# Kernel tuning notes

Hardware: AMD Instinct MI355X
Metric: run time of the kernel (lower is better)

## Reference

```python
import jax, jax.numpy as jnp
import numpy as np

V, E, H, ENC, ATT = 10000, 256, 512, 512, 512
B, S, NF, MAXLEN = 128, 25, 196, 64


def setup_inputs() -> dict:
    key = jax.random.key(0)
    ks = jax.random.split(key, 24)
    g = lambda k, shp: (jax.random.normal(k, shp, dtype=jnp.float32) * 0.05)
    emb = g(ks[0], (V, E)).at[0].set(0.0)  # padding_idx=0 row zeroed
    return {
        'decoder_input': jax.random.randint(ks[1], (B, S), 0, V, dtype=jnp.int32),
        'encoder_outputs': jax.random.normal(ks[2], (B, NF, ENC), dtype=jnp.float32),
        'emb': emb,
        'pos_emb': g(ks[3], (MAXLEN, E)),
        'Uw': g(ks[4], (ATT, ENC)), 'Ub': g(ks[5], (ATT,)),
        'Ww': g(ks[6], (ATT, H)), 'Wb': g(ks[7], (ATT,)),
        'Aw': g(ks[8], (1, ATT)), 'Ab': g(ks[9], (1,)),
        'init_h_w': g(ks[10], (H, ENC)), 'init_h_b': g(ks[11], (H,)),
        'init_c_w': g(ks[12], (H, ENC)), 'init_c_b': g(ks[13], (H,)),
        'W_ih': g(ks[14], (4 * H, E + ENC)), 'W_hh': g(ks[15], (4 * H, H)),
        'b_ih': g(ks[16], (4 * H,)), 'b_hh': g(ks[17], (4 * H,)),
        'fcn_w': g(ks[18], (V, H)), 'fcn_b': g(ks[19], (V,)),
    }


def reference(decoder_input, encoder_outputs, emb, pos_emb, Uw, Ub, Ww, Wb, Aw, Ab,
              init_h_w, init_h_b, init_c_w, init_c_b, W_ih, W_hh, b_ih, b_hh,
              fcn_w, fcn_b):
    # Loop-invariant attention key projection: U(features) -> [B, NF, ATT]
    u_hs = jnp.einsum('bne,ae->bna', encoder_outputs, Uw) + Ub
    mean_enc = encoder_outputs.mean(axis=1)                  # [B, ENC]
    h0 = mean_enc @ init_h_w.T + init_h_b                    # [B, H]
    c0 = mean_enc @ init_c_w.T + init_c_b
    tokens = decoder_input.T                                 # [S, B]
    positions = jnp.arange(tokens.shape[0])

    def step(carry, inp):
        h, c = carry
        tok, pos = inp
        embeds = emb[tok] + pos_emb[pos]                     # [B, E]
        w_ah = h @ Ww.T + Wb                                 # [B, ATT]
        scores = jnp.tanh(u_hs + w_ah[:, None, :]) @ Aw[0] + Ab[0]  # [B, NF]
        alpha = jax.nn.softmax(scores, axis=1)
        context = jnp.einsum('bnd,bn->bd', encoder_outputs, alpha)  # [B, ENC]
        x = jnp.concatenate([embeds, context], axis=1)       # [B, E+ENC]
        gates = x @ W_ih.T + b_ih + h @ W_hh.T + b_hh        # [B, 4H]
        i, f, g_, o = jnp.split(gates, 4, axis=1)
        c_new = jax.nn.sigmoid(f) * c + jax.nn.sigmoid(i) * jnp.tanh(g_)
        h_new = jax.nn.sigmoid(o) * jnp.tanh(c_new)
        out = h_new @ fcn_w.T + fcn_b                        # [B, V] (dropout=eval identity)
        return (h_new, c_new), (out, alpha)

    _, (outs, alphas) = jax.lax.scan(step, (h0, c0), (tokens, positions))
    return outs.transpose(1, 0, 2), alphas.transpose(1, 0, 2)
```

## Files before the change

### kernel.cpp

```cpp
#include <hip/hip_runtime.h>

constexpr int B_ = 128, S_ = 25, NF_ = 196, ENC_ = 512, ATT_ = 512;
constexpr int H_ = 512, E_ = 256, V_ = 10000, G4_ = 2048;
constexpr int VPAD_ = 10112;

typedef __attribute__((ext_vector_type(8))) __bf16 bf16x8;
typedef __attribute__((ext_vector_type(4))) __bf16 bf16x4;
typedef __attribute__((ext_vector_type(4))) float f32x4;

__device__ __forceinline__ float bflo(unsigned u) {
    return __builtin_bit_cast(float, u << 16);
}
__device__ __forceinline__ float bfhi(unsigned u) {
    return __builtin_bit_cast(float, u & 0xffff0000u);
}
__device__ __forceinline__ float fast_tanhf(float x) {
    x = fminf(fmaxf(x, -15.f), 15.f);
    return 1.f - 2.f * __fdividef(1.f, __expf(2.f * x) + 1.f);
}
__device__ __forceinline__ float fast_sigf(float x) {
    x = fminf(fmaxf(x, -30.f), 30.f);
    return __fdividef(1.f, 1.f + __expf(-x));
}

__device__ __forceinline__ int gperm(int n) {
    int j = (n & 15) + ((n >> 6) << 4);
    int g = (n >> 4) & 3;
    return g * 512 + j;
}

__global__ __launch_bounds__(256) void k_cvt(const float* __restrict__ s,
                                             __bf16* __restrict__ d, int n4) {
    int i = blockIdx.x * 256 + threadIdx.x;
    if (i >= n4) return;
    float4 v = *(const float4*)&s[(size_t)i * 4];
    bf16x4 o;
    o[0] = (__bf16)v.x; o[1] = (__bf16)v.y; o[2] = (__bf16)v.z; o[3] = (__bf16)v.w;
    *(bf16x4*)&d[(size_t)i * 4] = o;
}

__global__ __launch_bounds__(256) void k_cvt_fcw(const float* __restrict__ s,
                                                 __bf16* __restrict__ d) {
    int i = blockIdx.x * 256 + threadIdx.x;
    if (i >= VPAD_ * 512 / 4) return;
    int e = i * 4;
    int row = e >> 9;
    bf16x4 o;
    if (row < V_) {
        float4 v = *(const float4*)&s[(size_t)row * 512 + (e & 511)];
        o[0] = (__bf16)v.x; o[1] = (__bf16)v.y; o[2] = (__bf16)v.z; o[3] = (__bf16)v.w;
    } else {
        o[0] = o[1] = o[2] = o[3] = (__bf16)0.f;
    }
    *(bf16x4*)&d[(size_t)e] = o;
}

__global__ __launch_bounds__(256) void k_pack_ww(const float* __restrict__ Ww,
                                                 unsigned* __restrict__ W2) {
    __shared__ float Ts[32][65];
    int t = threadIdx.x;
    int k0 = blockIdx.x * 32, j0 = blockIdx.y * 64;
    int c = t & 31, rr = t >> 5;
#pragma unroll
    for (int i = 0; i < 8; ++i) {
        int j = j0 + rr + i * 8;
        Ts[c][rr + i * 8] = Ww[(size_t)j * 512 + k0 + c];
    }
    __syncthreads();
#pragma unroll
    for (int i = 0; i < 4; ++i) {
        int kr = (t >> 5) + i * 8;
        int jc = t & 31;
        __bf16 b0 = (__bf16)Ts[kr][2 * jc], b1 = (__bf16)Ts[kr][2 * jc + 1];
        unsigned u = (unsigned)__builtin_bit_cast(unsigned short, b0)
                   | ((unsigned)__builtin_bit_cast(unsigned short, b1) << 16);
        W2[(size_t)(k0 + kr) * 256 + (j0 >> 1) + jc] = u;
    }
}

__global__ __launch_bounds__(256) void k_cvt_wih_r(const float* __restrict__ W_ih,
                                                   __bf16* __restrict__ o) {
    int n = blockIdx.x, k = threadIdx.x;
    int row = gperm(n);
    o[(size_t)n * 256 + k] = (__bf16)W_ih[(size_t)row * 768 + k];
}

__global__ __launch_bounds__(256) void k_pack_wcat(const float* __restrict__ W_ih,
                                                   const float* __restrict__ W_hh,
                                                   __bf16* __restrict__ Wcat) {
    int n = blockIdx.x, t = threadIdx.x;
    int row = gperm(n);
#pragma unroll
    for (int i = 0; i < 4; ++i) {
        int k = t + i * 256;
        float v = (k < 512) ? W_ih[(size_t)row * 768 + 256 + k]
                            : W_hh[(size_t)row * 512 + (k - 512)];
        Wcat[(size_t)n * 1024 + k] = (__bf16)v;
    }
}

__global__ __launch_bounds__(256) void k_pack_biasr(const float* __restrict__ b_ih,
                                                    const float* __restrict__ b_hh,
                                                    float* __restrict__ bsum_r) {
    int n = blockIdx.x * 256 + threadIdx.x;
    int row = gperm(n);
    bsum_r[n] = b_ih[row] + b_hh[row];
}

__global__ __launch_bounds__(256) void k_embed(const int* __restrict__ dec,
                                               const float* __restrict__ emb,
                                               const float* __restrict__ pose,
                                               __bf16* __restrict__ out) {
    int bx = blockIdx.x;
    int s = bx >> 7, b = bx & 127;
    int e = threadIdx.x;
    int tok = dec[b * S_ + s];
    out[(size_t)bx * E_ + e] = (__bf16)(emb[tok * E_ + e] + pose[s * E_ + e]);
}

__global__ __launch_bounds__(1024) void k_init2(const float* __restrict__ enc,
                                                const float* __restrict__ ihw, const float* __restrict__ ihb,
                                                const float* __restrict__ icw, const float* __restrict__ icb,
                                                __bf16* __restrict__ Abuf0, float* __restrict__ cbuf) {
    __shared__ float pm[1024];
    __shared__ __align__(16) float mean[512];
    int b = blockIdx.x, t = threadIdx.x;
    int d = t & 511, q = t >> 9;
    const float* ep = enc + ((size_t)b * 196 + q * 98) * 512 + d;
    float sum = 0.f;
#pragma unroll 7
    for (int n = 0; n < 98; ++n) sum += ep[(size_t)n * 512];
    pm[t] = sum;
    __syncthreads();
    if (t < 512) mean[t] = (pm[t] + pm[t + 512]) * (1.f / 196.f);
    __syncthreads();
    int w = t >> 6, ln = t & 63;
    float4 m4a = *(const float4*)&mean[ln * 8];
    float4 m4b = *(const float4*)&mean[ln * 8 + 4];
#pragma unroll 4
    for (int i = 0; i < 32; ++i) {
        int j = i * 16 + w;
        const float4* wh = (const float4*)&ihw[(size_t)j * 512 + ln * 8];
        const float4* wc = (const float4*)&icw[(size_t)j * 512 + ln * 8];
        float4 ha = wh[0], hb = wh[1], ca = wc[0], cb = wc[1];
        float ah = m4a.x * ha.x + m4a.y * ha.y + m4a.z * ha.z + m4a.w * ha.w
                 + m4b.x * hb.x + m4b.y * hb.y + m4b.z * hb.z + m4b.w * hb.w;
        float ac = m4a.x * ca.x + m4a.y * ca.y + m4a.z * ca.z + m4a.w * ca.w
                 + m4b.x * cb.x + m4b.y * cb.y + m4b.z * cb.z + m4b.w * cb.w;
#pragma unroll
        for (int off = 32; off; off >>= 1) {
            ah += __shfl_xor(ah, off);
            ac += __shfl_xor(ac, off);
        }
        if (ln == 0) {
            Abuf0[(size_t)b * 1024 + 512 + j] = (__bf16)(ah + ihb[j]);
            cbuf[b * 512 + j] = ac + icb[j];
        }
    }
}

template<int MODE>
__global__ __launch_bounds__(256) void k_mfma_gemm(
    const __bf16* __restrict__ A, int lda, const __bf16* __restrict__ Bm,
    const float* __restrict__ bias1, void* __restrict__ Cout,
    int K, int Nreal, int ldc) {
    __shared__ __align__(16) __bf16 As[128 * 64];
    __shared__ __align__(16) __bf16 Bs[128 * 64];
    int tid = threadIdx.x;
    int lane = tid & 63, w = tid >> 6;
    int m0 = blockIdx.x * 128, n0 = blockIdx.y * 128;
    int wm = (w & 1) * 64, wn = (w >> 1) * 64;
    f32x4 acc[4][4] = {};
    int srow = tid >> 3;
    int ke = (tid & 7) * 8;
    int kgw = tid & 7;

    for (int k0 = 0; k0 < K; k0 += 64) {
#pragma unroll
        for (int it = 0; it < 4; ++it) {
            int row = it * 32 + srow;
            bf16x8 av = *(const bf16x8*)(A + (size_t)(m0 + row) * lda + k0 + ke);
            bf16x8 bv = *(const bf16x8*)(Bm + (size_t)(n0 + row) * K + k0 + ke);
            int kg = kgw ^ (row & 7);
            *(bf16x8*)&As[row * 64 + kg * 8] = av;
            *(bf16x8*)&Bs[row * 64 + kg * 8] = bv;
        }
        __syncthreads();
        bf16x8 af[4][2], bfr[4][2];
#pragma unroll
        for (int f = 0; f < 4; ++f) {
#pragma unroll
            for (int ks = 0; ks < 2; ++ks) {
                int ra = wm + f * 16 + (lane & 15);
                int rb = wn + f * 16 + (lane & 15);
                int kgl = ks * 4 + (lane >> 4);
                af[f][ks]  = *(const bf16x8*)&As[ra * 64 + (kgl ^ (ra & 7)) * 8];
                bfr[f][ks] = *(const bf16x8*)&Bs[rb * 64 + (kgl ^ (rb & 7)) * 8];
            }
        }
#pragma unroll
        for (int fm = 0; fm < 4; ++fm)
#pragma unroll
            for (int fn = 0; fn < 4; ++fn)
#pragma unroll
                for (int ks = 0; ks < 2; ++ks)
                    acc[fm][fn] = __builtin_amdgcn_mfma_f32_16x16x32_bf16(
                        af[fm][ks], bfr[fn][ks], acc[fm][fn], 0, 0, 0);
        __syncthreads();
    }
    int cm = (lane >> 4) * 4, cn = lane & 15;
#pragma unroll
    for (int fm = 0; fm < 4; ++fm) {
#pragma unroll
        for (int fn = 0; fn < 4; ++fn) {
#pragma unroll
            for (int r = 0; r < 4; ++r) {
                int gm = m0 + wm + fm * 16 + cm + r;
                int gn = n0 + wn + fn * 16 + cn;
                float v = acc[fm][fn][r];
                if (MODE == 0) {
                    if (gn < Nreal) {
                        int orow = (gm & 127) * S_ + (gm >> 7);
                        ((float*)Cout)[(size_t)orow * ldc + gn] = v + bias1[gn];
                    }
                } else {
                    ((__bf16*)Cout)[(size_t)gm * ldc + gn] = (__bf16)(v + bias1[gn]);
                }
            }
        }
    }
}

__global__ __launch_bounds__(1024) void k_attn2(
    const __bf16* __restrict__ u_hs,
    const unsigned* __restrict__ enc2,
    const unsigned* __restrict__ W2,
    const float* __restrict__ Wb, const float* __restrict__ Aw,
    __bf16* __restrict__ Abuf,
    float* __restrict__ alphas, int s) {
    __shared__ __align__(16) float hs[512];
    __shared__ float wah[512];
    __shared__ float pc[2048];
    __shared__ float sc[200];
    __shared__ float red[256];
    __shared__ float al[200];
    int b = blockIdx.x, t = threadIdx.x;
    int ln = t & 63, w = t >> 6;

    if (t < 256) {
        unsigned u = ((const unsigned*)Abuf)[b * 512 + 256 + t];
        hs[2 * t] = bflo(u); hs[2 * t + 1] = bfhi(u);
    }
    __syncthreads();
    {
        int jp = t & 255, kq = t >> 8;
        float a0 = 0.f, a1 = 0.f;
        const unsigned* wp = W2 + (size_t)(kq * 128) * 256 + jp;
        const float4* h4 = (const float4*)(hs + kq * 128);
#pragma unroll 4
        for (int k4 = 0; k4 < 32; ++k4) {
            float4 hk = h4[k4];
            unsigned w0 = wp[(k4 * 4 + 0) * 256];
            unsigned w1 = wp[(k4 * 4 + 1) * 256];
            unsigned w2 = wp[(k4 * 4 + 2) * 256];
            unsigned w3 = wp[(k4 * 4 + 3) * 256];
            a0 += hk.x * bflo(w0); a1 += hk.x * bfhi(w0);
            a0 += hk.y * bflo(w1); a1 += hk.y * bfhi(w1);
            a0 += hk.z * bflo(w2); a1 += hk.z * bfhi(w2);
            a0 += hk.w * bflo(w3); a1 += hk.w * bfhi(w3);
        }
        pc[kq * 512 + 2 * jp] = a0;
        pc[kq * 512 + 2 * jp + 1] = a1;
    }
    __syncthreads();
    if (t < 512)
        wah[t] = pc[t] + pc[512 + t] + pc[1024 + t] + pc[1536 + t] + Wb[t];
    __syncthreads();
    {
        float av[8], wv[8];
#pragma unroll
        for (int i = 0; i < 8; ++i) { av[i] = Aw[ln * 8 + i]; wv[i] = wah[ln * 8 + i]; }
        for (int n = w; n < NF_; n += 16) {
            bf16x8 u8 = *(const bf16x8*)(u_hs + ((size_t)(b * NF_ + n)) * 512 + ln * 8);
            float acc = 0.f;
#pragma unroll
            for (int i = 0; i < 8; ++i)
                acc += fast_tanhf((float)u8[i] + wv[i]) * av[i];
#pragma unroll
            for (int off = 32; off; off >>= 1) acc += __shfl_xor(acc, off);
            if (ln == 0) sc[n] = acc;
        }
    }
    __syncthreads();
    if (t < 256) red[t] = (t < NF_) ? sc[t] : -1e30f;
    __syncthreads();
#pragma unroll
    for (int off = 128; off; off >>= 1) {
        if (t < off) red[t] = fmaxf(red[t], red[t + off]);
        __syncthreads();
    }
    float mx = red[0];
    __syncthreads();
    float e = (t < NF_) ? __expf(sc[t] - mx) : 0.f;
    if (t < 256) red[t] = e;
    __syncthreads();
#pragma unroll
    for (int off = 128; off; off >>= 1) {
        if (t < off) red[t] += red[t + off];
        __syncthreads();
    }
    float inv = __fdividef(1.f, red[0]);
    __syncthreads();
    if (t < NF_) {
        float a = e * inv;
        al[t] = a;
        alphas[((size_t)b * S_ + s) * NF_ + t] = a;
    }
    __syncthreads();
    {
        int p2 = t & 255, q2 = t >> 8;
        float c0 = 0.f, c1 = 0.f;
        for (int i = q2; i < NF_; i += 4) {
            unsigned u = enc2[((size_t)(b * NF_ + i)) * 256 + p2];
            float a = al[i];
            c0 += a * bflo(u); c1 += a * bfhi(u);
        }
        pc[q2 * 512 + 2 * p2] = c0;
        pc[q2 * 512 + 2 * p2 + 1] = c1;
    }
    __syncthreads();
    if (t < 512)
        Abuf[(size_t)b * 1024 + t] =
            (__bf16)(pc[t] + pc[512 + t] + pc[1024 + t] + pc[1536 + t]);
}

__global__ __launch_bounds__(256) void k_gates(
    const __bf16* __restrict__ Abuf,
    const __bf16* __restrict__ Wcat,
    const __bf16* __restrict__ gatespre,
    float* __restrict__ cbuf,
    __bf16* __restrict__ AbufN,
    __bf16* __restrict__ Hall_bf,
    int s) {
    __shared__ __align__(16) __bf16 As[2][32 * 64];
    __shared__ __align__(16) __bf16 Bs[2][64 * 64];
    __shared__ float Red[2048];
    int tid = threadIdx.x;
    int lane = tid & 63, w = tid >> 6;
    int m0 = blockIdx.x * 32, n0 = blockIdx.y * 64;
    int kh = w >> 1, wm = (w & 1) * 16;
    f32x4 acc[4] = {};
    int srow = tid >> 3;
    int ke = (tid & 7) * 8;
    int kgw = tid & 7;

    for (int k0 = 0; k0 < 512; k0 += 64) {
#pragma unroll
        for (int h = 0; h < 2; ++h) {
            int kb = h * 512 + k0;
            bf16x8 av = *(const bf16x8*)(Abuf + (size_t)(m0 + srow) * 1024 + kb + ke);
            int kg = kgw ^ (srow & 7);
            *(bf16x8*)&As[h][srow * 64 + kg * 8] = av;
#pragma unroll
            for (int it = 0; it < 2; ++it) {
                int row = it * 32 + srow;
                bf16x8 bv = *(const bf16x8*)(Wcat + (size_t)(n0 + row) * 1024 + kb + ke);
                int kg2 = kgw ^ (row & 7);
                *(bf16x8*)&Bs[h][row * 64 + kg2 * 8] = bv;
            }
        }
        __syncthreads();
        bf16x8 af[2], bfr[4][2];
#pragma unroll
        for (int ks = 0; ks < 2; ++ks) {
            int ra = wm + (lane & 15);
            int kgl = ks * 4 + (lane >> 4);
            af[ks] = *(const bf16x8*)&As[kh][ra * 64 + ((kgl ^ (ra & 7))) * 8];
#pragma unroll
            for (int fn = 0; fn < 4; ++fn) {
                int rb = fn * 16 + (lane & 15);
                bfr[fn][ks] = *(const bf16x8*)&Bs[kh][rb * 64 + ((kgl ^ (rb & 7))) * 8];
            }
        }
#pragma unroll
        for (int fn = 0; fn < 4; ++fn)
#pragma unroll
            for (int ks = 0; ks < 2; ++ks)
                acc[fn] = __builtin_amdgcn_mfma_f32_16x16x32_bf16(
                    af[ks], bfr[fn][ks], acc[fn], 0, 0, 0);
        __syncthreads();
    }
    int base = ((w & 1) * 64 + lane) * 16;
    if (kh == 1) {
#pragma unroll
        for (int fn = 0; fn < 4; ++fn)
#pragma unroll
            for (int r = 0; r < 4; ++r) Red[base + fn * 4 + r] = acc[fn][r];
    }
    __syncthreads();
    if (kh == 0) {
#pragma unroll
        for (int fn = 0; fn < 4; ++fn)
#pragma unroll
            for (int r = 0; r < 4; ++r) acc[fn][r] += Red[base + fn * 4 + r];
        int cm = (lane >> 4) * 4, cn = lane & 15;
        int j = (n0 >> 6) * 16 + cn;
#pragma unroll
        for (int r = 0; r < 4; ++r) {
            int b = m0 + wm + cm + r;
            const __bf16* gp = gatespre + ((size_t)(s * B_ + b)) * G4_ + n0 + cn;
            float qi = acc[0][r] + (float)gp[0];
            float qf = acc[1][r] + (float)gp[16];
            float qg = acc[2][r] + (float)gp[32];
            float qo = acc[3][r] + (float)gp[48];
            float ig = fast_sigf(qi), fg = fast_sigf(qf);
            float gg = fast_tanhf(qg), og = fast_sigf(qo);
            int ci = b * 512 + j;
            float cnew = fg * cbuf[ci] + ig * gg;
            float hn = og * fast_tanhf(cnew);
            cbuf[ci] = cnew;
            __bf16 hb = (__bf16)hn;
            AbufN[(size_t)b * 1024 + 512 + j] = hb;
            Hall_bf[(size_t)(s + 1) * 65536 + ci] = hb;
        }
    }
}

extern "C" void kernel_launch(void* const* d_in, const int* in_sizes, int n_in,
                              void* d_out, int out_size, void* d_ws, size_t ws_size,
                              hipStream_t stream) {
    const int*   dec  = (const int*)d_in[0];
    const float* enc  = (const float*)d_in[1];
    const float* emb  = (const float*)d_in[2];
    const float* pose = (const float*)d_in[3];
    const float* Uw   = (const float*)d_in[4];
    const float* Ub   = (const float*)d_in[5];
    const float* Ww   = (const float*)d_in[6];
    const float* Wb   = (const float*)d_in[7];
    const float* Aw   = (const float*)d_in[8];
    const float* ihw  = (const float*)d_in[10];
    const float* ihb  = (const float*)d_in[11];
    const float* icw  = (const float*)d_in[12];
    const float* icb  = (const float*)d_in[13];
    const float* W_ih = (const float*)d_in[14];
    const float* W_hh = (const float*)d_in[15];
    const float* b_ih = (const float*)d_in[16];
    const float* b_hh = (const float*)d_in[17];
    const float* fcw  = (const float*)d_in[18];
    const float* fcb  = (const float*)d_in[19];
    float* out = (float*)d_out;
    char*  wsb = (char*)d_ws;

    size_t o = 0;
    __bf16*   enc_bf   = (__bf16*)(wsb + o); o += (size_t)25088 * 512 * 2;
    __bf16*   u_hs_bf  = (__bf16*)(wsb + o); o += (size_t)25088 * 512 * 2;
    __bf16*   gpre_bf  = (__bf16*)(wsb + o); o += (size_t)3200 * 2048 * 2;
    __bf16*   Hall_bf  = (__bf16*)(wsb + o); o += (size_t)26 * 65536 * 2;
    float*    cbuf     = (float*)(wsb + o);  o += (size_t)65536 * 4;
    __bf16*   Abuf     = (__bf16*)(wsb + o); o += (size_t)2 * 128 * 1024 * 2;
    __bf16*   Uw_bf    = (__bf16*)(wsb + o); o += (size_t)262144 * 2;
    unsigned* W2       = (unsigned*)(wsb + o); o += (size_t)512 * 256 * 4;
    __bf16*   WihE_r   = (__bf16*)(wsb + o); o += (size_t)2048 * 256 * 2;
    __bf16*   embeds_bf= (__bf16*)(wsb + o); o += (size_t)3200 * 256 * 2;
    __bf16*   Wcat     = (__bf16*)(wsb + o); o += (size_t)2048 * 1024 * 2;
    float*    bsum_r   = (float*)(wsb + o);  o += (size_t)2048 * 4;
    __bf16*   fcw_bf   = (__bf16*)(wsb + o); o += (size_t)VPAD_ * 512 * 2;

    k_cvt<<<12544, 256, 0, stream>>>(enc, enc_bf, 3211264);
    k_cvt<<<256, 256, 0, stream>>>(Uw, Uw_bf, 65536);
    k_pack_ww<<<dim3(16, 8), 256, 0, stream>>>(Ww, W2);
    k_cvt_wih_r<<<2048, 256, 0, stream>>>(W_ih, WihE_r);
    k_pack_wcat<<<2048, 256, 0, stream>>>(W_ih, W_hh, Wcat);
    k_pack_biasr<<<8, 256, 0, stream>>>(b_ih, b_hh, bsum_r);
    k_embed<<<S_ * B_, 256, 0, stream>>>(dec, emb, pose, embeds_bf);
    k_init2<<<B_, 1024, 0, stream>>>(enc, ihw, ihb, icw, icb, Abuf, cbuf);
    k_cvt_fcw<<<5056, 256, 0, stream>>>(fcw, fcw_bf);

    k_mfma_gemm<1><<<dim3(196, 4), 256, 0, stream>>>(enc_bf, 512, Uw_bf, Ub,
                                                     u_hs_bf, 512, 512, 512);
    k_mfma_gemm<1><<<dim3(25, 16), 256, 0, stream>>>(embeds_bf, 256, WihE_r, bsum_r,
                                                     gpre_bf, 256, 2048, 2048);

    for (int s = 0; s < S_; ++s) {
        __bf16* Ap = Abuf + (size_t)(s & 1) * 131072;
        __bf16* An = Abuf + (size_t)((s + 1) & 1) * 131072;
        k_attn2<<<B_, 1024, 0, stream>>>(u_hs_bf, (const unsigned*)enc_bf, W2, Wb, Aw,
                                         Ap, out + 32000000, s);
        k_gates<<<dim3(4, 32), 256, 0, stream>>>(Ap, Wcat, gpre_bf, cbuf, An, Hall_bf, s);
    }

    k_mfma_gemm<0><<<dim3(25, 79), 256, 0, stream>>>(Hall_bf + 65536, 512, fcw_bf, fcb,
                                                     out, 512, V_, V_);
}
```

Measured before the change: 1.426 ms.

## Split attention over feature halves with deferred softmax normalization in gates kernel

The attention kernel is split across two blocks per batch row, each handling 98 features with 512 threads. The softmax max-reduction is dropped: each block writes unnormalized exp scores, partial sums and partial context vectors. The gates kernel then combines the two halves, normalizes the context and alphas, and loads the context directly into shared memory. This removes the serial max/sum reduction barriers and doubles the block count for the latency-bound attention step. The trade-offs are a redundant W·h projection in both blocks, extra global traffic for the partial results, and overflow risk from computing exp without subtracting the max.

```diff
diff --git a/kernel.cpp b/kernel.cpp
--- a/kernel.cpp
+++ b/kernel.cpp
@@ -231,20 +231,20 @@
     }
 }
 
-__global__ __launch_bounds__(1024) void k_attn2(
+__global__ __launch_bounds__(512) void k_attn3(
     const __bf16* __restrict__ u_hs,
     const unsigned* __restrict__ enc2,
     const unsigned* __restrict__ W2,
     const float* __restrict__ Wb, const float* __restrict__ Aw,
-    __bf16* __restrict__ Abuf,
-    float* __restrict__ alphas, int s) {
+    const __bf16* __restrict__ Abuf,
+    float* __restrict__ pctx,
+    float* __restrict__ lpart,
+    float* __restrict__ esg) {
     __shared__ __align__(16) float hs[512];
     __shared__ float wah[512];
-    __shared__ float pc[2048];
-    __shared__ float sc[200];
-    __shared__ float red[256];
-    __shared__ float al[200];
-    int b = blockIdx.x, t = threadIdx.x;
+    __shared__ float pc[1024];
+    __shared__ float es[100];
+    int b = blockIdx.x, hh = blockIdx.y, t = threadIdx.x;
     int ln = t & 63, w = t >> 6;
 
     if (t < 256) {
@@ -253,12 +253,12 @@
     }
     __syncthreads();
     {
-        int jp = t & 255, kq = t >> 8;
+        int jp = t & 255, q = t >> 8;
         float a0 = 0.f, a1 = 0.f;
-        const unsigned* wp = W2 + (size_t)(kq * 128) * 256 + jp;
-        const float4* h4 = (const float4*)(hs + kq * 128);
+        const unsigned* wp = W2 + (size_t)(q * 256) * 256 + jp;
+        const float4* h4 = (const float4*)(hs + q * 256);
 #pragma unroll 4
-        for (int k4 = 0; k4 < 32; ++k4) {
+        for (int k4 = 0; k4 < 64; ++k4) {
             float4 hk = h4[k4];
             unsigned w0 = wp[(k4 * 4 + 0) * 256];
             unsigned w1 = wp[(k4 * 4 + 1) * 256];
@@ -269,18 +269,18 @@
             a0 += hk.z * bflo(w2); a1 += hk.z * bfhi(w2);
             a0 += hk.w * bflo(w3); a1 += hk.w * bfhi(w3);
         }
-        pc[kq * 512 + 2 * jp] = a0;
-        pc[kq * 512 + 2 * jp + 1] = a1;
-    }
-    __syncthreads();
-    if (t < 512)
-        wah[t] = pc[t] + pc[512 + t] + pc[1024 + t] + pc[1536 + t] + Wb[t];
+        pc[q * 512 + 2 * jp] = a0;
+        pc[q * 512 + 2 * jp + 1] = a1;
+    }
+    __syncthreads();
+    wah[t] = pc[t] + pc[512 + t] + Wb[t];
     __syncthreads();
     {
         float av[8], wv[8];
 #pragma unroll
         for (int i = 0; i < 8; ++i) { av[i] = Aw[ln * 8 + i]; wv[i] = wah[ln * 8 + i]; }
-        for (int n = w; n < NF_; n += 16) {
+        for (int nl = w; nl < 98; nl += 8) {
+            int n = hh * 98 + nl;
             bf16x8 u8 = *(const bf16x8*)(u_hs + ((size_t)(b * NF_ + n)) * 512 + ln * 8);
             float acc = 0.f;
 #pragma unroll
@@ -288,85 +288,90 @@
                 acc += fast_tanhf((float)u8[i] + wv[i]) * av[i];
 #pragma unroll
             for (int off = 32; off; off >>= 1) acc += __shfl_xor(acc, off);
-            if (ln == 0) sc[n] = acc;
-        }
-    }
-    __syncthreads();
-    if (t < 256) red[t] = (t < NF_) ? sc[t] : -1e30f;
-    __syncthreads();
-#pragma unroll
-    for (int off = 128; off; off >>= 1) {
-        if (t < off) red[t] = fmaxf(red[t], red[t + off]);
-        __syncthreads();
-    }
-    float mx = red[0];
-    __syncthreads();
-    float e = (t < NF_) ? __expf(sc[t] - mx) : 0.f;
-    if (t < 256) red[t] = e;
-    __syncthreads();
-#pragma unroll
-    for (int off = 128; off; off >>= 1) {
-        if (t < off) red[t] += red[t + off];
-        __syncthreads();
-    }
-    float inv = __fdividef(1.f, red[0]);
-    __syncthreads();
-    if (t < NF_) {
-        float a = e * inv;
-        al[t] = a;
-        alphas[((size_t)b * S_ + s) * NF_ + t] = a;
+            if (ln == 0) es[nl] = __expf(acc);
+        }
     }
     __syncthreads();
     {
         int p2 = t & 255, q2 = t >> 8;
         float c0 = 0.f, c1 = 0.f;
-        for (int i = q2; i < NF_; i += 4) {
-            unsigned u = enc2[((size_t)(b * NF_ + i)) * 256 + p2];
-            float a = al[i];
+        for (int i = q2; i < 98; i += 2) {
+            unsigned u = enc2[((size_t)(b * NF_ + hh * 98 + i)) * 256 + p2];
+            float a = es[i];
             c0 += a * bflo(u); c1 += a * bfhi(u);
         }
         pc[q2 * 512 + 2 * p2] = c0;
         pc[q2 * 512 + 2 * p2 + 1] = c1;
     }
     __syncthreads();
-    if (t < 512)
-        Abuf[(size_t)b * 1024 + t] =
-            (__bf16)(pc[t] + pc[512 + t] + pc[1024 + t] + pc[1536 + t]);
-}
-
-__global__ __launch_bounds__(256) void k_gates(
+    pctx[((size_t)(hh * 128 + b)) * 512 + t] = pc[t] + pc[512 + t];
+    if (t < 98) esg[b * 256 + hh * 98 + t] = es[t];
+    if (t < 64) {
+        float v = es[t] + ((t + 64 < 98) ? es[t + 64] : 0.f);
+#pragma unroll
+        for (int off = 32; off; off >>= 1) v += __shfl_xor(v, off);
+        if (t == 0) lpart[hh * 128 + b] = v;
+    }
+}
+
+__global__ __launch_bounds__(256) void k_gates2(
     const __bf16* __restrict__ Abuf,
     const __bf16* __restrict__ Wcat,
     const __bf16* __restrict__ gatespre,
     float* __restrict__ cbuf,
     __bf16* __restrict__ AbufN,
     __bf16* __restrict__ Hall_bf,
-    int s) {
-    __shared__ __align__(16) __bf16 As[2][32 * 64];
+    const float* __restrict__ pctx, const float* __restrict__ lpart,
+    const float* __restrict__ esg, float* __restrict__ alphas, int s) {
+    __shared__ __align__(16) __bf16 ctxL[32 * 512];
+    __shared__ __align__(16) __bf16 As[32 * 64];
     __shared__ __align__(16) __bf16 Bs[2][64 * 64];
     __shared__ float Red[2048];
+    __shared__ float invs[32];
     int tid = threadIdx.x;
     int lane = tid & 63, w = tid >> 6;
     int m0 = blockIdx.x * 32, n0 = blockIdx.y * 64;
     int kh = w >> 1, wm = (w & 1) * 16;
-    f32x4 acc[4] = {};
     int srow = tid >> 3;
     int ke = (tid & 7) * 8;
     int kgw = tid & 7;
 
+    if (tid < 32) invs[tid] = __fdividef(1.f, lpart[m0 + tid] + lpart[128 + m0 + tid]);
+    __syncthreads();
+    for (int q = tid; q < 8192; q += 256) {
+        int row = q >> 8;
+        int kk = (q & 255) * 2;
+        float2 v0 = *(const float2*)&pctx[((size_t)(m0 + row)) * 512 + kk];
+        float2 v1 = *(const float2*)&pctx[((size_t)(128 + m0 + row)) * 512 + kk];
+        float iv = invs[row];
+        int base = row * 512 + (kk & ~63) + ((((kk >> 3) & 7) ^ (row & 7)) << 3) + (kk & 7);
+        ctxL[base] = (__bf16)((v0.x + v1.x) * iv);
+        ctxL[base + 1] = (__bf16)((v0.y + v1.y) * iv);
+    }
+    if (blockIdx.y == 0) {
+        for (int q = tid; q < 32 * 256; q += 256) {
+            int row = q >> 8, n = q & 255;
+            if (n < NF_)
+                alphas[((size_t)(m0 + row) * S_ + s) * NF_ + n] =
+                    esg[(m0 + row) * 256 + n] * invs[row];
+        }
+    }
+    __syncthreads();
+
+    f32x4 acc[4] = {};
     for (int k0 = 0; k0 < 512; k0 += 64) {
-#pragma unroll
-        for (int h = 0; h < 2; ++h) {
-            int kb = h * 512 + k0;
-            bf16x8 av = *(const bf16x8*)(Abuf + (size_t)(m0 + srow) * 1024 + kb + ke);
-            int kg = kgw ^ (srow & 7);
-            *(bf16x8*)&As[h][srow * 64 + kg * 8] = av;
-#pragma unroll
-            for (int it = 0; it < 2; ++it) {
-                int row = it * 32 + srow;
-                bf16x8 bv = *(const bf16x8*)(Wcat + (size_t)(n0 + row) * 1024 + kb + ke);
-                int kg2 = kgw ^ (row & 7);
-                *(bf16x8*)&Bs[h][row * 64 + kg2 * 8] = bv;
+        {
+            bf16x8 av = *(const bf16x8*)(Abuf + (size_t)(m0 + srow) * 1024 + 512 + k0 + ke);
+            *(bf16x8*)&As[srow * 64 + (kgw ^ (srow & 7)) * 8] = av;
+#pragma unroll
+            for (int h = 0; h < 2; ++h) {
+                int kb = h * 512 + k0;
+#pragma unroll
+                for (int it = 0; it < 2; ++it) {
+                    int row = it * 32 + srow;
+                    bf16x8 bv = *(const bf16x8*)(Wcat + (size_t)(n0 + row) * 1024 + kb + ke);
+                    *(bf16x8*)&Bs[h][row * 64 + (kgw ^ (row & 7)) * 8] = bv;
+                }
             }
         }
         __syncthreads();
@@ -375,7 +380,10 @@
         for (int ks = 0; ks < 2; ++ks) {
             int ra = wm + (lane & 15);
             int kgl = ks * 4 + (lane >> 4);
-            af[ks] = *(const bf16x8*)&As[kh][ra * 64 + ((kgl ^ (ra & 7))) * 8];
+            if (kh == 0)
+                af[ks] = *(const bf16x8*)&ctxL[ra * 512 + k0 + ((kgl ^ (ra & 7))) * 8];
+            else
+                af[ks] = *(const bf16x8*)&As[ra * 64 + ((kgl ^ (ra & 7))) * 8];
 #pragma unroll
             for (int fn = 0; fn < 4; ++fn) {
                 int rb = fn * 16 + (lane & 15);
@@ -465,6 +473,9 @@
     __bf16*   Wcat     = (__bf16*)(wsb + o); o += (size_t)2048 * 1024 * 2;
     float*    bsum_r   = (float*)(wsb + o);  o += (size_t)2048 * 4;
     __bf16*   fcw_bf   = (__bf16*)(wsb + o); o += (size_t)VPAD_ * 512 * 2;
+    float*    pctx     = (float*)(wsb + o);  o += (size_t)2 * 128 * 512 * 4;
+    float*    lpart    = (float*)(wsb + o);  o += (size_t)256 * 4;
+    float*    esg      = (float*)(wsb + o);  o += (size_t)128 * 256 * 4;
 
     k_cvt<<<12544, 256, 0, stream>>>(enc, enc_bf, 3211264);
     k_cvt<<<256, 256, 0, stream>>>(Uw, Uw_bf, 65536);
@@ -484,9 +495,10 @@
     for (int s = 0; s < S_; ++s) {
         __bf16* Ap = Abuf + (size_t)(s & 1) * 131072;
         __bf16* An = Abuf + (size_t)((s + 1) & 1) * 131072;
-        k_attn2<<<B_, 1024, 0, stream>>>(u_hs_bf, (const unsigned*)enc_bf, W2, Wb, Aw,
-                                         Ap, out + 32000000, s);
-        k_gates<<<dim3(4, 32), 256, 0, stream>>>(Ap, Wcat, gpre_bf, cbuf, An, Hall_bf, s);
+        k_attn3<<<dim3(B_, 2), 512, 0, stream>>>(u_hs_bf, (const unsigned*)enc_bf, W2,
+                                                 Wb, Aw, Ap, pctx, lpart, esg);
+        k_gates2<<<dim3(4, 32), 256, 0, stream>>>(Ap, Wcat, gpre_bf, cbuf, An, Hall_bf,
+                                                  pctx, lpart, esg, out + 32000000, s);
     }
 
     k_mfma_gemm<0><<<dim3(25, 79), 256, 0, stream>>>(Hall_bf + 65536, 512, fcw_bf, fcb,
```

After: 1.765 ms. 23.7% more time.

## Drop softmax max-subtraction and tree reductions; remap GEMM tiles across XCDs

Applied to the files above, without the earlier changes.

The attention kernel now exponentiates scores directly with no max subtraction. Each wavefront computes the softmax sum with shuffles, and the normalisation is deferred onto the context output. This removes two shared-memory tree reductions and many __syncthreads per step. Skipping the max is safe only while the scores stay small enough not to overflow, which holds for the bounded tanh·Aw sums here. Separately, MODE 0 GEMM blocks are remapped so that neighbouring tiles land on the same XCD, which is meant to improve L2 reuse.

```diff
diff --git a/kernel.cpp b/kernel.cpp
--- a/kernel.cpp
+++ b/kernel.cpp
@@ -168,7 +168,19 @@
     __shared__ __align__(16) __bf16 Bs[128 * 64];
     int tid = threadIdx.x;
     int lane = tid & 63, w = tid >> 6;
-    int m0 = blockIdx.x * 128, n0 = blockIdx.y * 128;
+    int m0, n0;
+    if (MODE == 0) {
+        int nwg = gridDim.x * gridDim.y;
+        int bid = blockIdx.y * gridDim.x + blockIdx.x;
+        int q = nwg >> 3, r = nwg & 7;
+        int xcd = bid & 7, lid = bid >> 3;
+        int wgid = (xcd < r) ? xcd * (q + 1) + lid : r * (q + 1) + (xcd - r) * q + lid;
+        m0 = (wgid % gridDim.x) * 128;
+        n0 = (wgid / gridDim.x) * 128;
+    } else {
+        m0 = blockIdx.x * 128;
+        n0 = blockIdx.y * 128;
+    }
     int wm = (w & 1) * 64, wn = (w >> 1) * 64;
     f32x4 acc[4][4] = {};
     int srow = tid >> 3;
@@ -242,8 +254,6 @@
     __shared__ float wah[512];
     __shared__ float pc[2048];
     __shared__ float sc[200];
-    __shared__ float red[256];
-    __shared__ float al[200];
     int b = blockIdx.x, t = threadIdx.x;
     int ln = t & 63, w = t >> 6;
 
@@ -288,41 +298,22 @@
                 acc += fast_tanhf((float)u8[i] + wv[i]) * av[i];
 #pragma unroll
             for (int off = 32; off; off >>= 1) acc += __shfl_xor(acc, off);
-            if (ln == 0) sc[n] = acc;
-        }
-    }
-    __syncthreads();
-    if (t < 256) red[t] = (t < NF_) ? sc[t] : -1e30f;
-    __syncthreads();
-#pragma unroll
-    for (int off = 128; off; off >>= 1) {
-        if (t < off) red[t] = fmaxf(red[t], red[t + off]);
-        __syncthreads();
-    }
-    float mx = red[0];
-    __syncthreads();
-    float e = (t < NF_) ? __expf(sc[t] - mx) : 0.f;
-    if (t < 256) red[t] = e;
-    __syncthreads();
-#pragma unroll
-    for (int off = 128; off; off >>= 1) {
-        if (t < off) red[t] += red[t + off];
-        __syncthreads();
-    }
-    float inv = __fdividef(1.f, red[0]);
-    __syncthreads();
-    if (t < NF_) {
-        float a = e * inv;
-        al[t] = a;
-        alphas[((size_t)b * S_ + s) * NF_ + t] = a;
-    }
-    __syncthreads();
+            if (ln == 0) sc[n] = __expf(acc);
+        }
+    }
+    __syncthreads();
+    float sum = sc[ln] + sc[ln + 64] + sc[ln + 128];
+    if (ln < 4) sum += sc[ln + 192];
+#pragma unroll
+    for (int off = 32; off; off >>= 1) sum += __shfl_xor(sum, off);
+    float inv = __fdividef(1.f, sum);
+    if (t < NF_) alphas[((size_t)b * S_ + s) * NF_ + t] = sc[t] * inv;
     {
         int p2 = t & 255, q2 = t >> 8;
         float c0 = 0.f, c1 = 0.f;
         for (int i = q2; i < NF_; i += 4) {
             unsigned u = enc2[((size_t)(b * NF_ + i)) * 256 + p2];
-            float a = al[i];
+            float a = sc[i];
             c0 += a * bflo(u); c1 += a * bfhi(u);
         }
         pc[q2 * 512 + 2 * p2] = c0;
@@ -331,7 +322,7 @@
     __syncthreads();
     if (t < 512)
         Abuf[(size_t)b * 1024 + t] =
-            (__bf16)(pc[t] + pc[512 + t] + pc[1024 + t] + pc[1536 + t]);
+            (__bf16)((pc[t] + pc[512 + t] + pc[1024 + t] + pc[1536 + t]) * inv);
 }
 
 __global__ __launch_bounds__(256) void k_gates(
```

After: 1.410 ms. Within noise of the previous version (-1.1%).
